# Optimization experiments

Measured on AMD Instinct MI355X. Metric: run time of the kernel, lower is better.

The kernel has to match this reference:

```python
import jax, jax.numpy as jnp
import numpy as np

D_MODEL = 1024
NHEAD = 16
HEAD_DIM = D_MODEL // NHEAD
B, T = 2, 2048


def setup_inputs() -> dict:
    key = jax.random.key(0)
    ks = jax.random.split(key, 11)
    s = 1.0 / np.sqrt(D_MODEL)
    inp = {
        'q': jax.random.normal(ks[0], (B, T, D_MODEL), jnp.float32),
        'k': jax.random.normal(ks[1], (B, T, D_MODEL), jnp.float32),
        'v': jax.random.normal(ks[2], (B, T, D_MODEL), jnp.float32),
        'Wq': jax.random.normal(ks[3], (D_MODEL, D_MODEL), jnp.float32) * s,
        'bq': jnp.zeros((D_MODEL,), jnp.float32),
        'Wk': jax.random.normal(ks[4], (D_MODEL, D_MODEL), jnp.float32) * s,
        'bk': jnp.zeros((D_MODEL,), jnp.float32),
        'Wv': jax.random.normal(ks[5], (D_MODEL, D_MODEL), jnp.float32) * s,
        'bv': jnp.zeros((D_MODEL,), jnp.float32),
        'Wo': jax.random.normal(ks[6], (D_MODEL, D_MODEL), jnp.float32) * s,
        'bo': jnp.zeros((D_MODEL,), jnp.float32),
    }
    return inp


def reference(q, k, v, Wq, bq, Wk, bk, Wv, bv, Wo, bo):
    scale = np.sqrt(HEAD_DIM).astype(np.float32)
    # projections (torch Linear: x @ W.T + b), split heads -> [B, H, T, Dh]
    def proj(x, W, b):
        y = jnp.einsum('btd,ed->bte', x, W) + b
        return y.reshape(B, T, NHEAD, HEAD_DIM).transpose(0, 2, 1, 3)
    qh = proj(q, Wq, bq)
    kh = proj(k, Wk, bk)
    vh = proj(v, Wv, bv)
    scores = jnp.einsum('bhqd,bhkd->bhqk', qh, kh) / scale  # [B,H,T,T]
    weights = jax.nn.softmax(scores, axis=-1)
    out = jnp.einsum('bhqk,bhkd->bhqd', weights, vh)        # [B,H,T,Dh]
    out = out.transpose(0, 2, 1, 3).reshape(B, T, D_MODEL)
    return jnp.einsum('btd,ed->bte', out, Wo) + bo
```

## Files before the change

kernel.cpp:

```cpp
#include <hip/hip_runtime.h>
#include <cstdint>
#include <cstddef>


#define D_MODEL 1024
#define NHEAD   16
#define HDIM    64
#define BATCH   2
#define SEQ     2048
#define BT      (BATCH * SEQ)

#define QSCALE 0.18033688011112043f

typedef __bf16 bf16;
typedef __bf16 bf16x8 __attribute__((ext_vector_type(8)));
typedef __bf16 bf16x4 __attribute__((ext_vector_type(4)));
typedef float  floatx4 __attribute__((ext_vector_type(4)));
typedef short  short4v __attribute__((ext_vector_type(4)));

#define MFMA16(a, b, c) __builtin_amdgcn_mfma_f32_16x16x32_bf16((a), (b), (c), 0, 0, 0)

__device__ __forceinline__ float fexp2(float x) {
  return __builtin_amdgcn_exp2f(x);
}

__device__ __forceinline__ void async_cp16(const bf16* g, bf16* l) {
  __builtin_amdgcn_global_load_lds(
      (__attribute__((address_space(1))) void*)(g),
      (__attribute__((address_space(3))) void*)(l), 16, 0, 0);
}

__global__ __launch_bounds__(256) void cvt7(
    const float* __restrict__ s0, const float* __restrict__ s1,
    const float* __restrict__ s2, const float* __restrict__ s3,
    const float* __restrict__ s4, const float* __restrict__ s5,
    const float* __restrict__ s6,
    bf16* __restrict__ d0, bf16* __restrict__ d1, bf16* __restrict__ d2,
    bf16* __restrict__ d3, bf16* __restrict__ d4, bf16* __restrict__ d5,
    bf16* __restrict__ d6)
{
  const float* src; bf16* dst; int n4;
  switch (blockIdx.y) {
    case 0:  src = s0; dst = d0; n4 = (BT * D_MODEL) / 4; break;
    case 1:  src = s1; dst = d1; n4 = (BT * D_MODEL) / 4; break;
    case 2:  src = s2; dst = d2; n4 = (BT * D_MODEL) / 4; break;
    case 3:  src = s3; dst = d3; n4 = (D_MODEL * D_MODEL) / 4; break;
    case 4:  src = s4; dst = d4; n4 = (D_MODEL * D_MODEL) / 4; break;
    case 5:  src = s5; dst = d5; n4 = (D_MODEL * D_MODEL) / 4; break;
    default: src = s6; dst = d6; n4 = (D_MODEL * D_MODEL) / 4; break;
  }
  int stride = gridDim.x * blockDim.x;
  for (int i = blockIdx.x * blockDim.x + threadIdx.x; i < n4; i += stride) {
    float4 f = ((const float4*)src)[i];
    bf16x4 h;
    h[0] = (bf16)f.x; h[1] = (bf16)f.y; h[2] = (bf16)f.z; h[3] = (bf16)f.w;
    ((bf16x4*)dst)[i] = h;
  }
}

__device__ __forceinline__ void gemm128_core(
    const bf16* __restrict__ A, const bf16* __restrict__ W,
    int m0, int n0, bf16* As, bf16* Bs, floatx4 acc[4][4])
{
  const int t = threadIdx.x;
  const int l = t & 63, w = t >> 6;
  const int quad = l >> 4, lr = l & 15;
  const int wm = (w >> 1) * 64, wn = (w & 1) * 64;

  floatx4 z = {0.f, 0.f, 0.f, 0.f};
#pragma unroll
  for (int i = 0; i < 4; i++)
#pragma unroll
    for (int j = 0; j < 4; j++) acc[i][j] = z;

  for (int kt = 0; kt < 1024; kt += 32) {
    __syncthreads();
#pragma unroll
    for (int i = 0; i < 2; i++) {
      int c = i * 256 + t;
      int row = c >> 2, ci = c & 3;
      async_cp16(A + (size_t)(m0 + row) * 1024 + kt + ci * 8,
                 As + (i * 256 + w * 64) * 8);
      async_cp16(W + (size_t)(n0 + row) * 1024 + kt + ci * 8,
                 Bs + (i * 256 + w * 64) * 8);
    }
    __syncthreads();

    bf16x8 af[4], bfr[4];
#pragma unroll
    for (int i = 0; i < 4; i++) {
      af[i]  = *(const bf16x8*)(As + (wm + i * 16 + lr) * 32 + quad * 8);
      bfr[i] = *(const bf16x8*)(Bs + (wn + i * 16 + lr) * 32 + quad * 8);
    }
#pragma unroll
    for (int i = 0; i < 4; i++)
#pragma unroll
      for (int j = 0; j < 4; j++)
        acc[i][j] = MFMA16(af[i], bfr[j], acc[i][j]);
  }
}

__global__ __launch_bounds__(256) void qkv_gemm(
    const bf16* __restrict__ qb, const bf16* __restrict__ kb, const bf16* __restrict__ vb,
    const bf16* __restrict__ wq, const bf16* __restrict__ wk, const bf16* __restrict__ wv,
    const float* __restrict__ biasq, const float* __restrict__ biask, const float* __restrict__ biasv,
    bf16* __restrict__ qh, bf16* __restrict__ kh, bf16* __restrict__ vt)
{
  __shared__ bf16 As[128 * 32];
  __shared__ bf16 Bs[128 * 32];
  const int zid = blockIdx.z;
  const bf16* A = (zid == 0) ? qb : ((zid == 1) ? kb : vb);
  const bf16* W = (zid == 0) ? wq : ((zid == 1) ? wk : wv);
  const float* bias = (zid == 0) ? biasq : ((zid == 1) ? biask : biasv);
  const int m0 = blockIdx.x * 128, n0 = blockIdx.y * 128;

  floatx4 acc[4][4];
  gemm128_core(A, W, m0, n0, As, Bs, acc);

  const int t = threadIdx.x, l = t & 63, w = t >> 6;
  const int quad = l >> 4, lr = l & 15;
  const int wm = (w >> 1) * 64, wn = (w & 1) * 64;
  const float sc = (zid == 0) ? QSCALE : 1.0f;

  if (zid < 2) {
    bf16* out = (zid == 0) ? qh : kh;
#pragma unroll
    for (int i = 0; i < 4; i++) {
      int mbase = m0 + wm + i * 16 + quad * 4;
      int b  = mbase >> 11;
      int tq = mbase & 2047;
#pragma unroll
      for (int j = 0; j < 4; j++) {
        int n = n0 + wn + j * 16 + lr;
        float bv = bias[n];
        int h = n >> 6, dh = n & 63;
        bf16* p = out + ((size_t)((b * NHEAD + h) * SEQ + tq)) * HDIM + dh;
#pragma unroll
        for (int r = 0; r < 4; r++)
          p[(size_t)r * HDIM] = (bf16)((acc[i][j][r] + bv) * sc);
      }
    }
  } else {
#pragma unroll
    for (int i = 0; i < 4; i++) {
      int mbase = m0 + wm + i * 16 + quad * 4;
      int b  = mbase >> 11;
      int tq = mbase & 2047;
#pragma unroll
      for (int j = 0; j < 4; j++) {
        int n = n0 + wn + j * 16 + lr;
        float bv = bias[n];
        int h = n >> 6, dh = n & 63;
        bf16x4 pk;
#pragma unroll
        for (int r = 0; r < 4; r++) pk[r] = (bf16)(acc[i][j][r] + bv);
        *(bf16x4*)(vt + ((size_t)((b * NHEAD + h) * HDIM + dh)) * SEQ + tq) = pk;
      }
    }
  }
}

__global__ __launch_bounds__(256, 2) void attn_fused(
    const bf16* __restrict__ qh, const bf16* __restrict__ kh,
    const bf16* __restrict__ vt, bf16* __restrict__ attn)
{
  __shared__ __align__(16) char smem[65536];

  const int t = threadIdx.x, l = t & 63, w = t >> 6;
  const int quad = l >> 4, lr = l & 15;

  const int hb  = blockIdx.y * 16 + blockIdx.x;
  const int j   = hb >> 3;
  const int bh  = (hb & 7) + ((j & 3) << 3);
  const int qt0 = (j >> 2) * 128;

  const bf16* qg = qh + (size_t)bh * SEQ * HDIM;
  const bf16* kg = kh + (size_t)bh * SEQ * HDIM;
  const bf16* vg = vt + (size_t)bh * HDIM * SEQ;

  const bf16* kseg[4];
  const bf16* vseg[4];
#pragma unroll
  for (int i = 0; i < 4; i++) {
    int s = w * 4 + i;
    int krow = s * 8 + (l >> 3);
    kseg[i] = kg + (size_t)krow * HDIM + (((l & 7) ^ (l >> 3)) * 8);
    int vrow = s * 4 + (l >> 4);
    vseg[i] = vg + (size_t)vrow * SEQ + (((l & 15) ^ (vrow & 15)) * 8);
  }

  bf16x8 qf[2][2];
#pragma unroll
  for (int g = 0; g < 2; g++)
#pragma unroll
    for (int ko = 0; ko < 2; ko++)
      qf[g][ko] = *(const bf16x8*)(qg + (size_t)(qt0 + w * 32 + g * 16 + lr) * HDIM
                                   + ko * 32 + quad * 8);

  const floatx4 zz = {0.f, 0.f, 0.f, 0.f};
  floatx4 Oacc[2][4];
#pragma unroll
  for (int g = 0; g < 2; g++)
#pragma unroll
    for (int dt = 0; dt < 4; dt++) Oacc[g][dt] = zz;
  floatx4 Racc[2] = {zz, zz};
  float mrow[2] = {-3.0e38f, -3.0e38f};

  bf16x8 ones8;
#pragma unroll
  for (int i = 0; i < 8; i++) ones8[i] = (bf16)1.0f;

  auto stage = [&](int buf, int kt) {
    bf16* Kb = (bf16*)(smem + buf * 32768);
    bf16* Vb = (bf16*)(smem + buf * 32768 + 16384);
    int off = kt * 128;
#pragma unroll
    for (int i = 0; i < 4; i++) {
      async_cp16(kseg[i] + (size_t)off * HDIM, Kb + (w * 4 + i) * 512);
      async_cp16(vseg[i] + off,                Vb + (w * 4 + i) * 512);
    }
  };

  stage(0, 0);

  for (int kt = 0; kt < 16; kt++) {
    const int p = kt & 1;
    __syncthreads();
    if (kt + 1 < 16) stage(1 - p, kt + 1);
    const bf16* Ks  = (const bf16*)(smem + p * 32768);
    const bf16* Vts = (const bf16*)(smem + p * 32768 + 16384);

    const bf16* krow0 = Ks + lr * 64 + ((quad ^ (lr & 7)) * 8);
    const bf16* krow1 = Ks + lr * 64 + (((quad + 4) ^ (lr & 7)) * 8);

    floatx4 s0[8], s1[8];
#pragma unroll
    for (int ni = 0; ni < 8; ni++) {
      bf16x8 k0 = *(const bf16x8*)(krow0 + ni * 1024);
      bf16x8 k1 = *(const bf16x8*)(krow1 + ni * 1024);
      floatx4 a0 = MFMA16(k0, qf[0][0], zz);
      floatx4 a1 = MFMA16(k0, qf[1][0], zz);
      a0 = MFMA16(k1, qf[0][1], a0);
      a1 = MFMA16(k1, qf[1][1], a1);
      s0[ni] = a0;
      s1[ni] = a1;
    }

    bf16x8 pk0[4], pk1[4];
#pragma unroll
    for (int g = 0; g < 2; g++) {
      floatx4* sg = g ? s1 : s0;
      bf16x8* pkg = g ? pk1 : pk0;

      float xm[8];
#pragma unroll
      for (int ni = 0; ni < 8; ni++) {
        float m01 = fmaxf(sg[ni][0], sg[ni][1]);
        xm[ni] = fmaxf(fmaxf(m01, sg[ni][2]), sg[ni][3]);
      }
      float rmax = fmaxf(fmaxf(xm[0], xm[1]), xm[2]);
      rmax = fmaxf(fmaxf(rmax, xm[3]), xm[4]);
      rmax = fmaxf(fmaxf(rmax, xm[5]), xm[6]);
      rmax = fmaxf(rmax, xm[7]);
      rmax = fmaxf(rmax, __shfl_xor(rmax, 16, 64));
      rmax = fmaxf(rmax, __shfl_xor(rmax, 32, 64));

      if (!__all(rmax - mrow[g] <= 8.0f)) {
        float mnew = fmaxf(mrow[g], rmax);
        float al = fexp2(mrow[g] - mnew);
        mrow[g] = mnew;
#pragma unroll
        for (int dt = 0; dt < 4; dt++)
#pragma unroll
          for (int r = 0; r < 4; r++) Oacc[g][dt][r] *= al;
#pragma unroll
        for (int r = 0; r < 4; r++) Racc[g][r] *= al;
      }

      const float m = mrow[g];
#pragma unroll
      for (int nip = 0; nip < 4; nip++) {
        bf16x8 pv;
#pragma unroll
        for (int r = 0; r < 4; r++) pv[r]     = (bf16)fexp2(sg[2*nip  ][r] - m);
#pragma unroll
        for (int r = 0; r < 4; r++) pv[4 + r] = (bf16)fexp2(sg[2*nip+1][r] - m);
        pkg[nip] = pv;
      }
    }

    const bf16* vbase = Vts + lr * 128 + (quad & 1) * 4;
#pragma unroll
    for (int nip = 0; nip < 4; nip++) {
      const bf16* vpA = vbase + ((((4 * nip)     + (quad >> 1)) ^ lr) * 8);
      const bf16* vpB = vbase + ((((4 * nip + 2) + (quad >> 1)) ^ lr) * 8);
      Racc[0] = MFMA16(ones8, pk0[nip], Racc[0]);
      Racc[1] = MFMA16(ones8, pk1[nip], Racc[1]);
#pragma unroll
      for (int dt = 0; dt < 4; dt++) {
        bf16x4 va = *(const bf16x4*)(vpA + dt * 2048);
        bf16x4 vb = *(const bf16x4*)(vpB + dt * 2048);
        bf16x8 vf8 = __builtin_shufflevector(va, vb, 0, 1, 2, 3, 4, 5, 6, 7);
        Oacc[0][dt] = MFMA16(vf8, pk0[nip], Oacc[0][dt]);
        Oacc[1][dt] = MFMA16(vf8, pk1[nip], Oacc[1][dt]);
      }
    }
  }

  bf16* Ost = (bf16*)smem;
#pragma unroll
  for (int g = 0; g < 2; g++) {
    float inv = 1.0f / Racc[g][0];
#pragma unroll
    for (int dt = 0; dt < 4; dt++) {
      bf16x4 ov;
#pragma unroll
      for (int r = 0; r < 4; r++) ov[r] = (bf16)(Oacc[g][dt][r] * inv);
      *(bf16x4*)(Ost + (size_t)(w * 32 + g * 16 + lr) * 72 + dt * 16 + quad * 4) = ov;
    }
  }
  __syncthreads();

  const int b = bh >> 4, h = bh & 15;
#pragma unroll
  for (int i = 0; i < 4; i++) {
    int c = t + 256 * i;
    int row = c >> 3, ci = c & 7;
    *(int4*)(attn + ((size_t)b * SEQ + qt0 + row) * D_MODEL + h * HDIM + ci * 8) =
        *(const int4*)(Ost + row * 72 + ci * 8);
  }
}

__global__ __launch_bounds__(256) void oproj_gemm(
    const bf16* __restrict__ attn, const bf16* __restrict__ wo,
    const float* __restrict__ bo, float* __restrict__ out)
{
  __shared__ bf16 As[128 * 32];
  __shared__ bf16 Bs[64 * 32];
  const int m0 = blockIdx.x * 128, n0 = blockIdx.y * 64;
  const int t = threadIdx.x, l = t & 63, w = t >> 6;
  const int quad = l >> 4, lr = l & 15;
  const int wm = (w >> 1) * 64, wn = (w & 1) * 32;

  floatx4 z = {0.f, 0.f, 0.f, 0.f};
  floatx4 acc[4][2];
#pragma unroll
  for (int i = 0; i < 4; i++)
#pragma unroll
    for (int j = 0; j < 2; j++) acc[i][j] = z;

  for (int kt = 0; kt < 1024; kt += 32) {
    __syncthreads();
#pragma unroll
    for (int i = 0; i < 2; i++) {
      int c = i * 256 + t;
      int row = c >> 2, ci = c & 3;
      async_cp16(attn + (size_t)(m0 + row) * 1024 + kt + ci * 8,
                 As + (i * 256 + w * 64) * 8);
    }
    {
      int row = t >> 2, ci = t & 3;
      async_cp16(wo + (size_t)(n0 + row) * 1024 + kt + ci * 8,
                 Bs + (w * 64) * 8);
    }
    __syncthreads();

    bf16x8 af[4], bfr[2];
#pragma unroll
    for (int i = 0; i < 4; i++)
      af[i]  = *(const bf16x8*)(As + (wm + i * 16 + lr) * 32 + quad * 8);
#pragma unroll
    for (int j = 0; j < 2; j++)
      bfr[j] = *(const bf16x8*)(Bs + (wn + j * 16 + lr) * 32 + quad * 8);
#pragma unroll
    for (int i = 0; i < 4; i++)
#pragma unroll
      for (int j = 0; j < 2; j++)
        acc[i][j] = MFMA16(af[i], bfr[j], acc[i][j]);
  }

#pragma unroll
  for (int i = 0; i < 4; i++) {
    int m = m0 + wm + i * 16 + quad * 4;
#pragma unroll
    for (int j = 0; j < 2; j++) {
      int n = n0 + wn + j * 16 + lr;
      float bv = bo[n];
      float* p = out + (size_t)m * D_MODEL + n;
#pragma unroll
      for (int r = 0; r < 4; r++)
        p[(size_t)r * D_MODEL] = acc[i][j][r] + bv;
    }
  }
}

extern "C" void kernel_launch(void* const* d_in, const int* in_sizes, int n_in,
                              void* d_out, int out_size, void* d_ws, size_t ws_size,
                              hipStream_t stream)
{
  const float* q  = (const float*)d_in[0];
  const float* k  = (const float*)d_in[1];
  const float* v  = (const float*)d_in[2];
  const float* Wq = (const float*)d_in[3];
  const float* bq = (const float*)d_in[4];
  const float* Wk = (const float*)d_in[5];
  const float* bk = (const float*)d_in[6];
  const float* Wv = (const float*)d_in[7];
  const float* bv = (const float*)d_in[8];
  const float* Wo = (const float*)d_in[9];
  const float* bo = (const float*)d_in[10];

  const size_t NQ = (size_t)BT * D_MODEL;
  const size_t NW = (size_t)D_MODEL * D_MODEL;

  bf16* p = (bf16*)d_ws;
  bf16* qb   = p; p += NQ;
  bf16* kb   = p; p += NQ;
  bf16* vb   = p; p += NQ;
  bf16* wqb  = p; p += NW;
  bf16* wkb  = p; p += NW;
  bf16* wvb  = p; p += NW;
  bf16* wob  = p; p += NW;
  bf16* qhp  = p; p += NQ;
  bf16* khp  = p; p += NQ;
  bf16* vtp  = p; p += NQ;
  bf16* attn = p; p += NQ;

  cvt7<<<dim3(1024, 7, 1), 256, 0, stream>>>(q, k, v, Wq, Wk, Wv, Wo,
                                             qb, kb, vb, wqb, wkb, wvb, wob);
  qkv_gemm<<<dim3(32, 8, 3), 256, 0, stream>>>(qb, kb, vb, wqb, wkb, wvb,
                                               bq, bk, bv, qhp, khp, vtp);
  attn_fused<<<dim3(16, 32, 1), 256, 0, stream>>>(qhp, khp, vtp, attn);
  oproj_gemm<<<dim3(32, 16, 1), 256, 0, stream>>>(attn, wob, bo, (float*)d_out);
}
```

Measured before the change: 215.5 us.

## Software-pipeline attention loop with 64-key tiles and a four-buffer ring

Halves the key/value tile to 64 keys and stages tiles into a four-slot shared-memory ring with a prefetch distance of two. Each iteration now runs QK^T for the current tile, P·V for the previous tile, then softmax, so matrix work overlaps the exp/max work and global loads. The K/V copy layout and swizzle change to match the smaller tile. The cost is twice as many loop iterations and barriers, and two copies in flight per wave.

```diff
diff --git a/kernel.cpp b/kernel.cpp
--- a/kernel.cpp
+++ b/kernel.cpp
@@ -178,15 +178,14 @@
   const bf16* kg = kh + (size_t)bh * SEQ * HDIM;
   const bf16* vg = vt + (size_t)bh * HDIM * SEQ;
 
-  const bf16* kseg[4];
-  const bf16* vseg[4];
-#pragma unroll
-  for (int i = 0; i < 4; i++) {
-    int s = w * 4 + i;
-    int krow = s * 8 + (l >> 3);
-    kseg[i] = kg + (size_t)krow * HDIM + (((l & 7) ^ (l >> 3)) * 8);
-    int vrow = s * 4 + (l >> 4);
-    vseg[i] = vg + (size_t)vrow * SEQ + (((l & 15) ^ (vrow & 15)) * 8);
+  const bf16* kseg[2];
+  const bf16* vseg[2];
+#pragma unroll
+  for (int i = 0; i < 2; i++) {
+    int s = w * 2 + i;
+    int row = s * 8 + (l >> 3);
+    kseg[i] = kg + (size_t)row * HDIM + (((l & 7) ^ (row & 7)) * 8);
+    vseg[i] = vg + (size_t)row * SEQ + (((l & 7) ^ (row & 7)) * 8);
   }
 
   bf16x8 qf[2][2];
@@ -211,31 +210,23 @@
   for (int i = 0; i < 8; i++) ones8[i] = (bf16)1.0f;
 
   auto stage = [&](int buf, int kt) {
-    bf16* Kb = (bf16*)(smem + buf * 32768);
-    bf16* Vb = (bf16*)(smem + buf * 32768 + 16384);
-    int off = kt * 128;
-#pragma unroll
-    for (int i = 0; i < 4; i++) {
-      async_cp16(kseg[i] + (size_t)off * HDIM, Kb + (w * 4 + i) * 512);
-      async_cp16(vseg[i] + off,                Vb + (w * 4 + i) * 512);
+    bf16* Kb = (bf16*)(smem + buf * 16384);
+    bf16* Vb = (bf16*)(smem + buf * 16384 + 8192);
+    int off = kt * 64;
+#pragma unroll
+    for (int i = 0; i < 2; i++) {
+      async_cp16(kseg[i] + (size_t)off * HDIM, Kb + (w * 2 + i) * 512);
+      async_cp16(vseg[i] + off,                Vb + (w * 2 + i) * 512);
     }
   };
 
-  stage(0, 0);
-
-  for (int kt = 0; kt < 16; kt++) {
-    const int p = kt & 1;
-    __syncthreads();
-    if (kt + 1 < 16) stage(1 - p, kt + 1);
-    const bf16* Ks  = (const bf16*)(smem + p * 32768);
-    const bf16* Vts = (const bf16*)(smem + p * 32768 + 16384);
-
+  floatx4 s0[4], s1[4];
+  auto QK = [&](int buf) {
+    const bf16* Ks = (const bf16*)(smem + buf * 16384);
     const bf16* krow0 = Ks + lr * 64 + ((quad ^ (lr & 7)) * 8);
     const bf16* krow1 = Ks + lr * 64 + (((quad + 4) ^ (lr & 7)) * 8);
-
-    floatx4 s0[8], s1[8];
-#pragma unroll
-    for (int ni = 0; ni < 8; ni++) {
+#pragma unroll
+    for (int ni = 0; ni < 4; ni++) {
       bf16x8 k0 = *(const bf16x8*)(krow0 + ni * 1024);
       bf16x8 k1 = *(const bf16x8*)(krow1 + ni * 1024);
       floatx4 a0 = MFMA16(k0, qf[0][0], zz);
@@ -245,23 +236,22 @@
       s0[ni] = a0;
       s1[ni] = a1;
     }
-
-    bf16x8 pk0[4], pk1[4];
+  };
+
+  bf16x8 pk0[2], pk1[2];
+  auto SM = [&]() {
 #pragma unroll
     for (int g = 0; g < 2; g++) {
       floatx4* sg = g ? s1 : s0;
       bf16x8* pkg = g ? pk1 : pk0;
 
-      float xm[8];
-#pragma unroll
-      for (int ni = 0; ni < 8; ni++) {
+      float xm[4];
+#pragma unroll
+      for (int ni = 0; ni < 4; ni++) {
         float m01 = fmaxf(sg[ni][0], sg[ni][1]);
         xm[ni] = fmaxf(fmaxf(m01, sg[ni][2]), sg[ni][3]);
       }
-      float rmax = fmaxf(fmaxf(xm[0], xm[1]), xm[2]);
-      rmax = fmaxf(fmaxf(rmax, xm[3]), xm[4]);
-      rmax = fmaxf(fmaxf(rmax, xm[5]), xm[6]);
-      rmax = fmaxf(rmax, xm[7]);
+      float rmax = fmaxf(fmaxf(xm[0], xm[1]), fmaxf(xm[2], xm[3]));
       rmax = fmaxf(rmax, __shfl_xor(rmax, 16, 64));
       rmax = fmaxf(rmax, __shfl_xor(rmax, 32, 64));
 
@@ -279,7 +269,7 @@
 
       const float m = mrow[g];
 #pragma unroll
-      for (int nip = 0; nip < 4; nip++) {
+      for (int nip = 0; nip < 2; nip++) {
         bf16x8 pv;
 #pragma unroll
         for (int r = 0; r < 4; r++) pv[r]     = (bf16)fexp2(sg[2*nip  ][r] - m);
@@ -288,24 +278,42 @@
         pkg[nip] = pv;
       }
     }
-
-    const bf16* vbase = Vts + lr * 128 + (quad & 1) * 4;
-#pragma unroll
-    for (int nip = 0; nip < 4; nip++) {
-      const bf16* vpA = vbase + ((((4 * nip)     + (quad >> 1)) ^ lr) * 8);
-      const bf16* vpB = vbase + ((((4 * nip + 2) + (quad >> 1)) ^ lr) * 8);
+  };
+
+  auto PV = [&](int buf) {
+    const bf16* Vts = (const bf16*)(smem + buf * 16384 + 8192);
+    const bf16* vbase = Vts + lr * 64 + (quad & 1) * 4;
+#pragma unroll
+    for (int nip = 0; nip < 2; nip++) {
+      const bf16* vpA = vbase + ((((4 * nip)     + (quad >> 1)) ^ (lr & 7)) * 8);
+      const bf16* vpB = vbase + ((((4 * nip + 2) + (quad >> 1)) ^ (lr & 7)) * 8);
       Racc[0] = MFMA16(ones8, pk0[nip], Racc[0]);
       Racc[1] = MFMA16(ones8, pk1[nip], Racc[1]);
 #pragma unroll
       for (int dt = 0; dt < 4; dt++) {
-        bf16x4 va = *(const bf16x4*)(vpA + dt * 2048);
-        bf16x4 vb = *(const bf16x4*)(vpB + dt * 2048);
+        bf16x4 va = *(const bf16x4*)(vpA + dt * 1024);
+        bf16x4 vb = *(const bf16x4*)(vpB + dt * 1024);
         bf16x8 vf8 = __builtin_shufflevector(va, vb, 0, 1, 2, 3, 4, 5, 6, 7);
         Oacc[0][dt] = MFMA16(vf8, pk0[nip], Oacc[0][dt]);
         Oacc[1][dt] = MFMA16(vf8, pk1[nip], Oacc[1][dt]);
       }
     }
-  }
+  };
+
+  stage(0, 0);
+  stage(1, 1);
+  __syncthreads();
+  stage(2, 2);
+  QK(0);
+  SM();
+  for (int kt = 1; kt < 32; kt++) {
+    __syncthreads();
+    if (kt + 2 < 32) stage((kt + 2) & 3, kt + 2);
+    QK(kt & 3);
+    PV((kt - 1) & 3);
+    SM();
+  }
+  PV(31 & 3);
 
   bf16* Ost = (bf16*)smem;
 #pragma unroll
```

Result: slower. 221.1 us (+2.6%).

## Software-pipeline attention loop to overlap QK^T of next tile with PV of previous

Applied to the files above, without the earlier changes.

Splits the attention inner loop into QK, softmax, V-load and PV stages and reorders them across iterations. The QK^T MFMAs for tile kt now run alongside the PV MFMAs for tile kt-1, and the V fragments are preloaded into registers before the buffer gets overwritten. The aim is to hide softmax/exp latency and LDS read latency behind matrix work. In exchange, score tiles, probabilities and 16 V fragments are live at the same time, which raises VGPR pressure and may lower occupancy. The change to the K swizzle expression is equivalent to the old one.

```diff
diff --git a/kernel.cpp b/kernel.cpp
--- a/kernel.cpp
+++ b/kernel.cpp
@@ -184,7 +184,7 @@
   for (int i = 0; i < 4; i++) {
     int s = w * 4 + i;
     int krow = s * 8 + (l >> 3);
-    kseg[i] = kg + (size_t)krow * HDIM + (((l & 7) ^ (l >> 3)) * 8);
+    kseg[i] = kg + (size_t)krow * HDIM + (((l & 7) ^ (krow & 7)) * 8);
     int vrow = s * 4 + (l >> 4);
     vseg[i] = vg + (size_t)vrow * SEQ + (((l & 15) ^ (vrow & 15)) * 8);
   }
@@ -221,19 +221,11 @@
     }
   };
 
-  stage(0, 0);
-
-  for (int kt = 0; kt < 16; kt++) {
-    const int p = kt & 1;
-    __syncthreads();
-    if (kt + 1 < 16) stage(1 - p, kt + 1);
-    const bf16* Ks  = (const bf16*)(smem + p * 32768);
-    const bf16* Vts = (const bf16*)(smem + p * 32768 + 16384);
-
+  floatx4 s0[8], s1[8];
+  auto QK = [&](int buf) {
+    const bf16* Ks = (const bf16*)(smem + buf * 32768);
     const bf16* krow0 = Ks + lr * 64 + ((quad ^ (lr & 7)) * 8);
     const bf16* krow1 = Ks + lr * 64 + (((quad + 4) ^ (lr & 7)) * 8);
-
-    floatx4 s0[8], s1[8];
 #pragma unroll
     for (int ni = 0; ni < 8; ni++) {
       bf16x8 k0 = *(const bf16x8*)(krow0 + ni * 1024);
@@ -245,8 +237,10 @@
       s0[ni] = a0;
       s1[ni] = a1;
     }
-
-    bf16x8 pk0[4], pk1[4];
+  };
+
+  bf16x8 pk0[4], pk1[4];
+  auto SM = [&]() {
 #pragma unroll
     for (int g = 0; g < 2; g++) {
       floatx4* sg = g ? s1 : s0;
@@ -288,24 +282,53 @@
         pkg[nip] = pv;
       }
     }
-
+  };
+
+  bf16x8 vreg[4][4];
+  auto VLOAD = [&](int buf) {
+    const bf16* Vts = (const bf16*)(smem + buf * 32768 + 16384);
     const bf16* vbase = Vts + lr * 128 + (quad & 1) * 4;
 #pragma unroll
     for (int nip = 0; nip < 4; nip++) {
       const bf16* vpA = vbase + ((((4 * nip)     + (quad >> 1)) ^ lr) * 8);
       const bf16* vpB = vbase + ((((4 * nip + 2) + (quad >> 1)) ^ lr) * 8);
-      Racc[0] = MFMA16(ones8, pk0[nip], Racc[0]);
-      Racc[1] = MFMA16(ones8, pk1[nip], Racc[1]);
 #pragma unroll
       for (int dt = 0; dt < 4; dt++) {
         bf16x4 va = *(const bf16x4*)(vpA + dt * 2048);
         bf16x4 vb = *(const bf16x4*)(vpB + dt * 2048);
-        bf16x8 vf8 = __builtin_shufflevector(va, vb, 0, 1, 2, 3, 4, 5, 6, 7);
-        Oacc[0][dt] = MFMA16(vf8, pk0[nip], Oacc[0][dt]);
-        Oacc[1][dt] = MFMA16(vf8, pk1[nip], Oacc[1][dt]);
-      }
-    }
-  }
+        vreg[nip][dt] = __builtin_shufflevector(va, vb, 0, 1, 2, 3, 4, 5, 6, 7);
+      }
+    }
+  };
+
+  auto PVR = [&]() {
+#pragma unroll
+    for (int nip = 0; nip < 4; nip++) {
+      Racc[0] = MFMA16(ones8, pk0[nip], Racc[0]);
+      Racc[1] = MFMA16(ones8, pk1[nip], Racc[1]);
+#pragma unroll
+      for (int dt = 0; dt < 4; dt++) {
+        Oacc[0][dt] = MFMA16(vreg[nip][dt], pk0[nip], Oacc[0][dt]);
+        Oacc[1][dt] = MFMA16(vreg[nip][dt], pk1[nip], Oacc[1][dt]);
+      }
+    }
+  };
+
+  stage(0, 0);
+  __syncthreads();
+  stage(1, 1);
+  QK(0);
+  VLOAD(0);
+  SM();
+  for (int kt = 1; kt < 16; kt++) {
+    __syncthreads();
+    if (kt + 1 < 16) stage((kt + 1) & 1, kt + 1);
+    QK(kt & 1);
+    PVR();
+    SM();
+    VLOAD(kt & 1);
+  }
+  PVR();
 
   bf16* Ost = (bf16*)smem;
 #pragma unroll
```

New measurement: 223.4 us. 1.04x slower.
